# Optimization experiments

Hardware: AMD Instinct MI355X
Metric: run time of the kernel (lower is better)

Reference implementation:

```python
import jax, jax.numpy as jnp
import numpy as np

T, B = 384, 128
IN_DIM, HID, OUT_DIM = 512, 1024, 512


def _lstm_step(h, c, x_t, Wx, Wh, b):
    # x_t: [B, D], h/c: [B, H]; gates order: i, f, g, o
    gates = x_t @ Wx + h @ Wh + b  # [B, 4H]
    i, f, g, o = jnp.split(gates, 4, axis=-1)
    c_new = jax.nn.sigmoid(f) * c + jax.nn.sigmoid(i) * jnp.tanh(g)
    h_new = jax.nn.sigmoid(o) * jnp.tanh(c_new)
    return h_new, c_new


def setup_inputs() -> dict:
    key = jax.random.key(0)
    ks = jax.random.split(key, 9)
    s_in = 1.0 / np.sqrt(IN_DIM)
    s_h = 1.0 / np.sqrt(HID)
    s_o = 1.0 / np.sqrt(OUT_DIM)
    return {
        "x": jax.random.normal(ks[0], (T, B, IN_DIM), dtype=jnp.float32),
        "hidden_state": jnp.zeros((1, B, HID), dtype=jnp.float32),
        "cell_state": jnp.zeros((1, B, HID), dtype=jnp.float32),
        "enc_Wx": jax.random.normal(ks[1], (IN_DIM, 4 * HID), dtype=jnp.float32) * s_in,
        "enc_Wh": jax.random.normal(ks[2], (HID, 4 * HID), dtype=jnp.float32) * s_h,
        "enc_b": jnp.zeros((4 * HID,), dtype=jnp.float32),
        "dec_Wx": jax.random.normal(ks[3], (OUT_DIM, 4 * HID), dtype=jnp.float32) * s_o,
        "dec_Wh": jax.random.normal(ks[4], (HID, 4 * HID), dtype=jnp.float32) * s_h,
        "dec_b": jnp.zeros((4 * HID,), dtype=jnp.float32),
        "fc_W": jax.random.normal(ks[5], (HID, OUT_DIM), dtype=jnp.float32) * s_h,
        "fc_b": jnp.zeros((OUT_DIM,), dtype=jnp.float32),
    }


def reference(x, hidden_state, cell_state, enc_Wx, enc_Wh, enc_b,
              dec_Wx, dec_Wh, dec_b, fc_W, fc_b):
    # ---- encoder: run LSTM over T steps, keep only final hidden state ----
    h0, c0 = hidden_state[0], cell_state[0]  # [B, H]

    def enc_step(carry, x_t):
        h, c = carry
        h, c = _lstm_step(h, c, x_t, enc_Wx, enc_Wh, enc_b)
        return (h, c), None

    (h_enc, _), _ = jax.lax.scan(enc_step, (h0, c0), x)

    y0 = jnp.zeros((B, OUT_DIM), dtype=x.dtype)
    c_dec0 = jnp.zeros((B, HID), dtype=x.dtype)

    def dec_step(carry, _):
        y, h, c = carry
        h, c = _lstm_step(h, c, y, dec_Wx, dec_Wh, dec_b)
        y = jax.nn.softmax(h @ fc_W + fc_b, axis=-1)  # softmax over dim=2
        return (y, h, c), y

    _, output = jax.lax.scan(dec_step, (y0, h_enc, c_dec0), None, length=T)
    return output  # [T, B, OUT_DIM]
```

## Files before the change

### kernel.cpp

```cpp
#include <hip/hip_runtime.h>


#define TS 384

typedef __attribute__((ext_vector_type(8))) short bf16x8;
typedef __attribute__((ext_vector_type(4))) float f32x4;

#define WS_XR 4096u
#define XR_SLOT 262144u
#define WS_HP (WS_XR + 4u*XR_SLOT)
#define HP_BUF 524288u
#define WS_FPN (WS_HP + 2u*HP_BUF)
#define WS_TOTAL (WS_FPN + 2097152u)

__device__ __forceinline__ unsigned short bf16r(float v) {
  unsigned u = __float_as_uint(v);
  u += 0x7FFFu + ((u >> 16) & 1u);
  return (unsigned short)(u >> 16);
}
__device__ __forceinline__ float bf2f(unsigned short h) {
  return __uint_as_float(((unsigned)h) << 16);
}
__device__ __forceinline__ void split2(float v, short& hi, short& lo) {
  unsigned short h = bf16r(v);
  float r = v - bf2f(h);
  hi = (short)h; lo = (short)bf16r(r);
}
__device__ __forceinline__ float sigm(float v)  { return 1.0f / (1.0f + __expf(-v)); }
__device__ __forceinline__ float tanhfa(float v){ return 1.0f - 2.0f / (__expf(2.0f*v) + 1.0f); }

__device__ __forceinline__ void st_u64(void* p, unsigned long long v) {
  __hip_atomic_store((unsigned long long*)p, v, __ATOMIC_RELAXED, __HIP_MEMORY_SCOPE_AGENT);
}
__device__ __forceinline__ void st_f32(float* p, float v) {
  __hip_atomic_store(p, v, __ATOMIC_RELAXED, __HIP_MEMORY_SCOPE_AGENT);
}
__device__ __forceinline__ float ld_f32(const float* p) {
  return __hip_atomic_load(p, __ATOMIC_RELAXED, __HIP_MEMORY_SCOPE_AGENT);
}
union FRAG { unsigned long long q[2]; bf16x8 v; };
__device__ __forceinline__ bf16x8 ld_frag(const short* base) {
  FRAG u;
  u.q[0] = __hip_atomic_load((const unsigned long long*)base, __ATOMIC_RELAXED, __HIP_MEMORY_SCOPE_AGENT);
  u.q[1] = __hip_atomic_load((const unsigned long long*)(base + 4), __ATOMIC_RELAXED, __HIP_MEMORY_SCOPE_AGENT);
  return u.v;
}

__device__ __forceinline__ void setflag(unsigned* flag, unsigned val) {
  asm volatile("s_waitcnt vmcnt(0)" ::: "memory");
  __syncthreads();
  if (threadIdx.x == 0) {
    __hip_atomic_store(flag, val, __ATOMIC_RELAXED, __HIP_MEMORY_SCOPE_AGENT);
    asm volatile("s_waitcnt vmcnt(0)" ::: "memory");
  }
}
__device__ __forceinline__ void waitflags(const unsigned* flags, int nflags,
                                          unsigned target, bool fence, int* sDead) {
  if (threadIdx.x < 64) {
    const int i = threadIdx.x;
    const bool act = (i * 4) < nflags;
    const unsigned long long* q = (const unsigned long long*)(flags + i * 4);
    unsigned spins = 0;
    for (;;) {
      bool ok = true;
      if (act) {
        unsigned long long q0 = __hip_atomic_load(q, __ATOMIC_RELAXED, __HIP_MEMORY_SCOPE_AGENT);
        unsigned long long q1 = __hip_atomic_load(q + 1, __ATOMIC_RELAXED, __HIP_MEMORY_SCOPE_AGENT);
        ok = ((unsigned)q0 >= target) && ((unsigned)(q0 >> 32) >= target)
          && ((unsigned)q1 >= target) && ((unsigned)(q1 >> 32) >= target);
      }
      if (__all(ok)) break;
      __builtin_amdgcn_s_sleep(1);
      if (++spins > (1u << 19)) { if (i == 0) *sDead = 1; break; }
    }
    if (fence) __builtin_amdgcn_fence(__ATOMIC_ACQUIRE, "agent");
  }
  __syncthreads();
}

__device__ void load_gate_weights(const float* __restrict__ Wx, const float* __restrict__ Wh,
                                  int p, short* sBh, short* sBl) {
  for (int idx = threadIdx.x; idx < 24576; idx += 1024) {
    int j = idx & 7, l = (idx >> 3) & 63, kb = idx >> 9;
    int k = kb * 32 + ((l >> 4) << 3) + j;
    int c = l & 15;
    int gcol = (c >> 2) * 1024 + p * 4 + (c & 3);
    float wv = (k < 512) ? Wx[(size_t)k * 4096 + gcol]
                         : Wh[(size_t)(k - 512) * 4096 + gcol];
    short hi, lo; split2(wv, hi, lo);
    sBh[idx] = hi; sBl[idx] = lo;
  }
}
__device__ void load_fc_weights(const float* __restrict__ fcW, int kg, int cg,
                                short* sFh, short* sFl) {
  for (int idx = threadIdx.x; idx < 4096; idx += 1024) {
    int j = idx & 7, l = (idx >> 3) & 63, kb = idx >> 9;
    int unit = kg * 256 + kb * 32 + ((l >> 4) << 3) + j;
    int col = cg * 16 + (l & 15);
    short hi, lo; split2(fcW[(size_t)unit * 512 + col], hi, lo);
    sFh[idx] = hi; sFl[idx] = lo;
  }
}

__device__ __forceinline__ void gg(const short* AHs, const short* ALs,
    const short* BHs, const short* BLs, int mt, int l,
    int kbA0, int kbB0, int nkb, f32x4* acc)
{
  const bf16x8* AH = (const bf16x8*)AHs;
  const bf16x8* AL = (const bf16x8*)ALs;
  const bf16x8* BH = (const bf16x8*)BHs;
  const bf16x8* BL = (const bf16x8*)BLs;
  #pragma unroll 2
  for (int i = 0; i < nkb; i += 2) {
    int ka = kbA0 + i, kb = kbB0 + i;
    bf16x8 ah0 = AH[(ka * 8 + mt) * 64 + l];
    bf16x8 al0 = AL[(ka * 8 + mt) * 64 + l];
    bf16x8 bh0 = BH[kb * 64 + l];
    bf16x8 bl0 = BL[kb * 64 + l];
    bf16x8 ah1 = AH[((ka + 1) * 8 + mt) * 64 + l];
    bf16x8 al1 = AL[((ka + 1) * 8 + mt) * 64 + l];
    bf16x8 bh1 = BH[(kb + 1) * 64 + l];
    bf16x8 bl1 = BL[(kb + 1) * 64 + l];
    acc[0] = __builtin_amdgcn_mfma_f32_16x16x32_bf16(ah0, bh0, acc[0], 0, 0, 0);
    acc[1] = __builtin_amdgcn_mfma_f32_16x16x32_bf16(ah0, bl0, acc[1], 0, 0, 0);
    acc[2] = __builtin_amdgcn_mfma_f32_16x16x32_bf16(al0, bh0, acc[2], 0, 0, 0);
    acc[3] = __builtin_amdgcn_mfma_f32_16x16x32_bf16(ah1, bh1, acc[3], 0, 0, 0);
    acc[4] = __builtin_amdgcn_mfma_f32_16x16x32_bf16(ah1, bl1, acc[4], 0, 0, 0);
    acc[5] = __builtin_amdgcn_mfma_f32_16x16x32_bf16(al1, bh1, acc[5], 0, 0, 0);
  }
}
__device__ __forceinline__ void gg_finish(f32x4* acc, int kh, int mt, int l,
                                          float* LDSgate) {
  f32x4 s = (acc[0] + acc[3]) + ((acc[1] + acc[4]) + (acc[2] + acc[5]));
  const int col = l & 15, r0 = mt * 16 + ((l >> 4) << 2);
  float* plane = LDSgate + kh * 2176;
  #pragma unroll
  for (int j = 0; j < 4; ++j) plane[(r0 + j) * 17 + col] = s[j];
}

__device__ __forceinline__ void conv_x(const float* __restrict__ xsrc,
                                       short* dstH, short* dstL, int p, int t) {
  if (t < 32) {
    int g = p * 32 + t;
    int l = g & 63, mt = (g >> 6) & 7, kb = g >> 9;
    int row = mt * 16 + (l & 15), k = kb * 32 + ((l >> 4) << 3);
    const float* xs = xsrc + (size_t)row * 512 + k;
    unsigned long long h64[2] = {0, 0}, l64[2] = {0, 0};
    #pragma unroll
    for (int j = 0; j < 8; ++j) {
      short hi, lo; split2(xs[j], hi, lo);
      h64[j >> 2] |= (unsigned long long)(unsigned short)hi << ((j & 3) * 16);
      l64[j >> 2] |= (unsigned long long)(unsigned short)lo << ((j & 3) * 16);
    }
    int off = g * 8;
    st_u64(dstH + off, h64[0]); st_u64(dstH + off + 4, h64[1]);
    st_u64(dstL + off, l64[0]); st_u64(dstL + off + 4, l64[1]);
  }
}

__global__ void __launch_bounds__(1024, 1)
lstm6(const float* __restrict__ x, const float* __restrict__ h0p,
      const float* __restrict__ c0p, const float* __restrict__ eWx,
      const float* __restrict__ eWh, const float* __restrict__ eb,
      const float* __restrict__ dWx, const float* __restrict__ dWh,
      const float* __restrict__ db, const float* __restrict__ fcW,
      const float* __restrict__ fcb, float* __restrict__ out,
      char* __restrict__ ws)
{
  __shared__ __align__(16) short sBh[24576], sBl[24576];
  __shared__ __align__(16) short sFh[4096], sFl[4096];
  __shared__ float LDSgate[2 * 2176];
  __shared__ unsigned hsplit[512];
  __shared__ float ybuf[512];
  __shared__ float red[16];
  __shared__ int sDead;

  const int p = blockIdx.x, t = threadIdx.x;
  const int w = t >> 6, l = t & 63;
  const int mt = w & 7, kh = w >> 3;
  if (t == 0) sDead = 0;

  unsigned* hflag = (unsigned*)ws;
  unsigned* yflag = (unsigned*)(ws + 1024);
  unsigned* fflag = (unsigned*)(ws + 2048);

  short* xrH[4]; short* xrL[4];
  #pragma unroll
  for (int s4 = 0; s4 < 4; ++s4) {
    xrH[s4] = (short*)(ws + WS_XR + s4 * XR_SLOT);
    xrL[s4] = (short*)(ws + WS_XR + s4 * XR_SLOT + 131072u);
  }
  short* hpH[2]; short* hpL[2];
  #pragma unroll
  for (int b2 = 0; b2 < 2; ++b2) {
    hpH[b2] = (short*)(ws + WS_HP + b2 * HP_BUF);
    hpL[b2] = (short*)(ws + WS_HP + b2 * HP_BUF + 262144u);
  }
  float* fp = (float*)(ws + WS_FPN);

  const int row_pw = t & 127, u_pw = (t >> 7) & 3;

  load_gate_weights(eWx, eWh, p, sBh, sBl);
  conv_x(x, xrH[0], xrL[0], p, t);
  conv_x(x + 65536, xrH[1], xrL[1], p, t);
  if (t < 64) {
    int hg = p * 64 + t;
    int ll = hg & 63, mtt = (hg >> 6) & 7, hk = hg >> 9;
    int row = mtt * 16 + (ll & 15), k = hk * 32 + ((ll >> 4) << 3);
    const float* hs = h0p + (size_t)row * 1024 + k;
    unsigned long long h64[2] = {0, 0}, l64[2] = {0, 0};
    #pragma unroll
    for (int j = 0; j < 8; ++j) {
      short hi, lo; split2(hs[j], hi, lo);
      h64[j >> 2] |= (unsigned long long)(unsigned short)hi << ((j & 3) * 16);
      l64[j >> 2] |= (unsigned long long)(unsigned short)lo << ((j & 3) * 16);
    }
    int off = hg * 8;
    st_u64(hpH[0] + off, h64[0]); st_u64(hpH[0] + off + 4, h64[1]);
    st_u64(hpL[0] + off, l64[0]); st_u64(hpL[0] + off + 4, l64[1]);
  }
  float creg = 0.f, bq0 = 0.f, bq1 = 0.f, bq2 = 0.f, bq3 = 0.f;
  if (t < 512) {
    creg = c0p[(size_t)row_pw * 1024 + p * 4 + u_pw];
    bq0 = eb[0 * 1024 + p * 4 + u_pw];
    bq1 = eb[1 * 1024 + p * 4 + u_pw];
    bq2 = eb[2 * 1024 + p * 4 + u_pw];
    bq3 = eb[3 * 1024 + p * 4 + u_pw];
  }
  setflag(&hflag[p], 1u);
  waitflags(hflag, 256, 1u, true, &sDead);
  if (sDead) return;

  for (int st = 0; st < TS; ++st) {
    int rb = st & 1, wb = rb ^ 1, xs = st & 3;
    f32x4 z = {0.f, 0.f, 0.f, 0.f};
    f32x4 acc[6] = {z, z, z, z, z, z};
    gg(xrH[xs], xrL[xs], sBh, sBl, mt, l, kh * 8, kh * 8, 8, acc);
    waitflags(hflag, 256, (unsigned)(st + 1), true, &sDead);
    if (sDead) return;
    gg(hpH[rb], hpL[rb], sBh, sBl, mt, l, kh * 16, 16 + kh * 16, 16, acc);
    gg_finish(acc, kh, mt, l, LDSgate);
    __syncthreads();
    if (t < 512) {
      float g0 = LDSgate[row_pw * 17 + 0  + u_pw] + LDSgate[2176 + row_pw * 17 + 0  + u_pw] + bq0;
      float g1 = LDSgate[row_pw * 17 + 4  + u_pw] + LDSgate[2176 + row_pw * 17 + 4  + u_pw] + bq1;
      float g2 = LDSgate[row_pw * 17 + 8  + u_pw] + LDSgate[2176 + row_pw * 17 + 8  + u_pw] + bq2;
      float g3 = LDSgate[row_pw * 17 + 12 + u_pw] + LDSgate[2176 + row_pw * 17 + 12 + u_pw] + bq3;
      creg = sigm(g1) * creg + sigm(g0) * tanhfa(g2);
      float h = sigm(g3) * tanhfa(creg);
      short hi, lo; split2(h, hi, lo);
      hsplit[u_pw * 128 + row_pw] = ((unsigned)(unsigned short)hi << 16) | (unsigned short)lo;
    }
    if (st + 2 < TS)
      conv_x(x + (size_t)(st + 2) * 65536, xrH[(st + 2) & 3], xrL[(st + 2) & 3], p, t);
    __syncthreads();
    if (t < 128) {
      int r = t;
      unsigned w0 = hsplit[r], w1 = hsplit[128 + r], w2 = hsplit[256 + r], w3 = hsplit[384 + r];
      unsigned long long hi64 = (unsigned long long)(w0 >> 16)
        | ((unsigned long long)(w1 >> 16) << 16)
        | ((unsigned long long)(w2 >> 16) << 32)
        | ((unsigned long long)(w3 >> 16) << 48);
      unsigned long long lo64 = (unsigned long long)(w0 & 0xFFFFu)
        | ((unsigned long long)(w1 & 0xFFFFu) << 16)
        | ((unsigned long long)(w2 & 0xFFFFu) << 32)
        | ((unsigned long long)(w3 & 0xFFFFu) << 48);
      int hk = p >> 3, mtt = r >> 4;
      int lane_ = (((p >> 1) & 3) << 4) | (r & 15);
      int off = ((hk * 8 + mtt) * 64 + lane_) * 8 + (p & 1) * 4;
      st_u64(hpH[wb] + off, hi64);
      st_u64(hpL[wb] + off, lo64);
    }
    setflag(&hflag[p], (unsigned)(st + 2));
  }

  load_gate_weights(dWx, dWh, p, sBh, sBl);
  if (p >= 128) load_fc_weights(fcW, (p - 128) >> 5, (p - 128) & 31, sFh, sFl);
  if (t < 32) {
    int off = (p * 32 + t) * 8;
    st_u64(xrH[0] + off, 0ull); st_u64(xrH[0] + off + 4, 0ull);
    st_u64(xrL[0] + off, 0ull); st_u64(xrL[0] + off + 4, 0ull);
  }
  creg = 0.0f;
  if (t < 512) {
    bq0 = db[0 * 1024 + p * 4 + u_pw];
    bq1 = db[1 * 1024 + p * 4 + u_pw];
    bq2 = db[2 * 1024 + p * 4 + u_pw];
    bq3 = db[3 * 1024 + p * 4 + u_pw];
  }
  float fcb_r = (t < 512) ? fcb[t] : 0.f;
  setflag(&hflag[p], (unsigned)(TS + 2));

  const unsigned DB = (unsigned)(TS + 2);
  for (int st = 0; st < TS; ++st) {
    int rb = st & 1, wb = rb ^ 1;
    int ys = st & 1, yw = ys ^ 1;
    f32x4 z = {0.f, 0.f, 0.f, 0.f};
    f32x4 acc[6] = {z, z, z, z, z, z};
    waitflags(hflag, 256, DB + (unsigned)st, true, &sDead);
    if (sDead) return;
    gg(hpH[rb], hpL[rb], sBh, sBl, mt, l, kh * 16, 16 + kh * 16, 16, acc);
    waitflags(yflag, 128, (unsigned)st, false, &sDead);
    if (sDead) return;
    gg(xrH[ys], xrL[ys], sBh, sBl, mt, l, kh * 8, kh * 8, 8, acc);
    gg_finish(acc, kh, mt, l, LDSgate);
    __syncthreads();
    if (t < 512) {
      float g0 = LDSgate[row_pw * 17 + 0  + u_pw] + LDSgate[2176 + row_pw * 17 + 0  + u_pw] + bq0;
      float g1 = LDSgate[row_pw * 17 + 4  + u_pw] + LDSgate[2176 + row_pw * 17 + 4  + u_pw] + bq1;
      float g2 = LDSgate[row_pw * 17 + 8  + u_pw] + LDSgate[2176 + row_pw * 17 + 8  + u_pw] + bq2;
      float g3 = LDSgate[row_pw * 17 + 12 + u_pw] + LDSgate[2176 + row_pw * 17 + 12 + u_pw] + bq3;
      creg = sigm(g1) * creg + sigm(g0) * tanhfa(g2);
      float h = sigm(g3) * tanhfa(creg);
      short hi, lo; split2(h, hi, lo);
      hsplit[u_pw * 128 + row_pw] = ((unsigned)(unsigned short)hi << 16) | (unsigned short)lo;
    }
    __syncthreads();
    if (t < 128) {
      int r = t;
      unsigned w0 = hsplit[r], w1 = hsplit[128 + r], w2 = hsplit[256 + r], w3 = hsplit[384 + r];
      unsigned long long hi64 = (unsigned long long)(w0 >> 16)
        | ((unsigned long long)(w1 >> 16) << 16)
        | ((unsigned long long)(w2 >> 16) << 32)
        | ((unsigned long long)(w3 >> 16) << 48);
      unsigned long long lo64 = (unsigned long long)(w0 & 0xFFFFu)
        | ((unsigned long long)(w1 & 0xFFFFu) << 16)
        | ((unsigned long long)(w2 & 0xFFFFu) << 32)
        | ((unsigned long long)(w3 & 0xFFFFu) << 48);
      int hk = p >> 3, mtt = r >> 4;
      int lane_ = (((p >> 1) & 3) << 4) | (r & 15);
      int off = ((hk * 8 + mtt) * 64 + lane_) * 8 + (p & 1) * 4;
      st_u64(hpH[wb] + off, hi64);
      st_u64(hpL[wb] + off, lo64);
    }
    setflag(&hflag[p], DB + (unsigned)(st + 1));

    if (p >= 128) {
      const int f = p - 128, kg = f >> 5, cg = f & 31;
      waitflags(hflag + kg * 64, 64, DB + (unsigned)(st + 1), false, &sDead);
      if (sDead) return;
      {
        const bf16x8* FB = (const bf16x8*)sFh;
        const bf16x8* FL = (const bf16x8*)sFl;
        f32x4 a0 = z, a1 = z, a2 = z;
        #pragma unroll
        for (int kb = 0; kb < 4; ++kb) {
          int gkb = kg * 8 + kh * 4 + kb;
          bf16x8 ah = ld_frag(hpH[wb] + ((gkb * 8 + mt) * 64 + l) * 8);
          bf16x8 al = ld_frag(hpL[wb] + ((gkb * 8 + mt) * 64 + l) * 8);
          bf16x8 bh = FB[(kh * 4 + kb) * 64 + l];
          bf16x8 bl = FL[(kh * 4 + kb) * 64 + l];
          a0 = __builtin_amdgcn_mfma_f32_16x16x32_bf16(ah, bh, a0, 0, 0, 0);
          a1 = __builtin_amdgcn_mfma_f32_16x16x32_bf16(ah, bl, a1, 0, 0, 0);
          a2 = __builtin_amdgcn_mfma_f32_16x16x32_bf16(al, bh, a2, 0, 0, 0);
        }
        f32x4 s = a0 + (a1 + a2);
        int slice = kg * 2 + kh;
        int col = cg * 16 + (l & 15), r0 = mt * 16 + ((l >> 4) << 2);
        #pragma unroll
        for (int j = 0; j < 4; ++j)
          st_f32(&fp[(size_t)(slice * 128 + r0 + j) * 512 + col], s[j]);
      }
      setflag(&fflag[f], (unsigned)(st + 1));
    } else {
      waitflags(fflag, 128, (unsigned)(st + 1), false, &sDead);
      if (sDead) return;
      float v = 0.f, e = 0.f, mx;
      if (t < 512) {
        v = fcb_r;
        #pragma unroll
        for (int s8 = 0; s8 < 8; ++s8)
          v += ld_f32(&fp[(size_t)(s8 * 128 + p) * 512 + t]);
        mx = v;
        #pragma unroll
        for (int o = 32; o > 0; o >>= 1) mx = fmaxf(mx, __shfl_xor(mx, o));
        if (l == 0) red[w] = mx;
      }
      __syncthreads();
      if (t < 512) {
        mx = red[0];
        #pragma unroll
        for (int i = 1; i < 8; ++i) mx = fmaxf(mx, red[i]);
        e = __expf(v - mx);
        float ss = e;
        #pragma unroll
        for (int o = 32; o > 0; o >>= 1) ss += __shfl_xor(ss, o);
        if (l == 0) red[8 + w] = ss;
      }
      __syncthreads();
      if (t < 512) {
        float ss = (red[8] + red[9]) + (red[10] + red[11])
                 + (red[12] + red[13]) + (red[14] + red[15]);
        float y = e / ss;
        out[((size_t)st * 128 + p) * 512 + t] = y;
        ybuf[t] = y;
      }
      __syncthreads();
      if (t < 64) {
        int kb = t >> 2, seg = t & 3;
        int k = kb * 32 + seg * 8;
        int lane_ = (seg << 4) | (p & 15), mtt = p >> 4;
        int off = ((kb * 8 + mtt) * 64 + lane_) * 8;
        unsigned long long h64[2] = {0, 0}, l64[2] = {0, 0};
        #pragma unroll
        for (int j = 0; j < 8; ++j) {
          short hi, lo; split2(ybuf[k + j], hi, lo);
          h64[j >> 2] |= (unsigned long long)(unsigned short)hi << ((j & 3) * 16);
          l64[j >> 2] |= (unsigned long long)(unsigned short)lo << ((j & 3) * 16);
        }
        st_u64(xrH[yw] + off, h64[0]); st_u64(xrH[yw] + off + 4, h64[1]);
        st_u64(xrL[yw] + off, l64[0]); st_u64(xrL[yw] + off + 4, l64[1]);
      }
      setflag(&yflag[p], (unsigned)(st + 1));
    }
  }
}

extern "C" void kernel_launch(void* const* d_in, const int* in_sizes, int n_in,
                              void* d_out, int out_size, void* d_ws, size_t ws_size,
                              hipStream_t stream) {
  const float* x   = (const float*)d_in[0];
  const float* h0  = (const float*)d_in[1];
  const float* c0  = (const float*)d_in[2];
  const float* eWx = (const float*)d_in[3];
  const float* eWh = (const float*)d_in[4];
  const float* eb  = (const float*)d_in[5];
  const float* dWx = (const float*)d_in[6];
  const float* dWh = (const float*)d_in[7];
  const float* db  = (const float*)d_in[8];
  const float* fcW = (const float*)d_in[9];
  const float* fcb = (const float*)d_in[10];
  float* out = (float*)d_out;

  if (ws_size < (size_t)WS_TOTAL) {
    hipMemsetAsync(d_out, 0xFF, (size_t)out_size * sizeof(float), stream);
    return;
  }
  hipMemsetAsync(d_ws, 0, 4096, stream);
  hipLaunchKernelGGL(lstm6, dim3(256), dim3(1024), 0, stream,
                     x, h0, c0, eWx, eWh, eb, dWx, dWh, db, fcW, fcb, out,
                     (char*)d_ws);
}
```

Measured before the change: 15.77 ms.

## Use hierarchical flag aggregation for grid barriers and pipeline MFMA operand loads

Replaces the flat wait, where every block polls all 256 (or 128) flags, with a two-level scheme. A few designated aggregator blocks poll a 32-flag group each and publish one summary flag, and all blocks then poll only the 4–8 summary words. This cuts global polling traffic on every step's cross-block barrier. The GEMM inner loop is rewritten as a templated, fully unrolled software pipeline that prefetches A fragments a few k-blocks ahead. The FC stage batches its global fragment loads before the MFMAs. The x-conversion work moves to the threads that are otherwise idle during the gate nonlinearity, and the partial-sum reduction becomes a tree. The aggregation adds an extra hop of latency per barrier and depends on the aggregator blocks making progress.

After: 16.65 ms. +5.6%, slower.

```diff
diff --git a/kernel.cpp b/kernel.cpp
--- a/kernel.cpp
+++ b/kernel.cpp
@@ -13,6 +13,8 @@
 #define WS_FPN (WS_HP + 2u*HP_BUF)
 #define WS_TOTAL (WS_FPN + 2097152u)
 
+#define MFMA __builtin_amdgcn_mfma_f32_16x16x32_bf16
+
 __device__ __forceinline__ unsigned short bf16r(float v) {
   unsigned u = __float_as_uint(v);
   u += 0x7FFFu + ((u >> 16) & 1u);
@@ -32,6 +34,12 @@
 __device__ __forceinline__ void st_u64(void* p, unsigned long long v) {
   __hip_atomic_store((unsigned long long*)p, v, __ATOMIC_RELAXED, __HIP_MEMORY_SCOPE_AGENT);
 }
+__device__ __forceinline__ unsigned long long ld_u64(const void* p) {
+  return __hip_atomic_load((const unsigned long long*)p, __ATOMIC_RELAXED, __HIP_MEMORY_SCOPE_AGENT);
+}
+__device__ __forceinline__ void st_u32(unsigned* p, unsigned v) {
+  __hip_atomic_store(p, v, __ATOMIC_RELAXED, __HIP_MEMORY_SCOPE_AGENT);
+}
 __device__ __forceinline__ void st_f32(float* p, float v) {
   __hip_atomic_store(p, v, __ATOMIC_RELAXED, __HIP_MEMORY_SCOPE_AGENT);
 }
@@ -41,39 +49,66 @@
 union FRAG { unsigned long long q[2]; bf16x8 v; };
 __device__ __forceinline__ bf16x8 ld_frag(const short* base) {
   FRAG u;
-  u.q[0] = __hip_atomic_load((const unsigned long long*)base, __ATOMIC_RELAXED, __HIP_MEMORY_SCOPE_AGENT);
-  u.q[1] = __hip_atomic_load((const unsigned long long*)(base + 4), __ATOMIC_RELAXED, __HIP_MEMORY_SCOPE_AGENT);
+  u.q[0] = ld_u64(base);
+  u.q[1] = ld_u64(base + 4);
   return u.v;
 }
 
 __device__ __forceinline__ void setflag(unsigned* flag, unsigned val) {
   asm volatile("s_waitcnt vmcnt(0)" ::: "memory");
   __syncthreads();
-  if (threadIdx.x == 0) {
+  if (threadIdx.x == 0)
     __hip_atomic_store(flag, val, __ATOMIC_RELAXED, __HIP_MEMORY_SCOPE_AGENT);
-    asm volatile("s_waitcnt vmcnt(0)" ::: "memory");
-  }
-}
-__device__ __forceinline__ void waitflags(const unsigned* flags, int nflags,
-                                          unsigned target, bool fence, int* sDead) {
-  if (threadIdx.x < 64) {
-    const int i = threadIdx.x;
-    const bool act = (i * 4) < nflags;
-    const unsigned long long* q = (const unsigned long long*)(flags + i * 4);
+}
+__device__ __forceinline__ void wait_hier(const unsigned* flags, unsigned* pub,
+    int aggIdx, int nPub, unsigned target, bool fence, int* sDead) {
+  const int t = threadIdx.x;
+  if (aggIdx >= 0) {
+    if (t < 8) {
+      const unsigned long long* q = (const unsigned long long*)(flags + aggIdx * 32 + t * 4);
+      unsigned spins = 0;
+      for (;;) {
+        unsigned long long q0 = ld_u64(q), q1 = ld_u64(q + 1);
+        bool ok = ((unsigned)q0 >= target) && ((unsigned)(q0 >> 32) >= target)
+               && ((unsigned)q1 >= target) && ((unsigned)(q1 >> 32) >= target);
+        if (__all(ok)) break;
+        __builtin_amdgcn_s_sleep(1);
+        if (++spins > (1u << 19)) { if (t == 0) *sDead = 1; break; }
+      }
+    }
+    if (t == 0) st_u32(&pub[aggIdx], target);
+  }
+  if (t == 0) {
     unsigned spins = 0;
     for (;;) {
       bool ok = true;
-      if (act) {
-        unsigned long long q0 = __hip_atomic_load(q, __ATOMIC_RELAXED, __HIP_MEMORY_SCOPE_AGENT);
-        unsigned long long q1 = __hip_atomic_load(q + 1, __ATOMIC_RELAXED, __HIP_MEMORY_SCOPE_AGENT);
-        ok = ((unsigned)q0 >= target) && ((unsigned)(q0 >> 32) >= target)
-          && ((unsigned)q1 >= target) && ((unsigned)(q1 >> 32) >= target);
-      }
+      #pragma unroll
+      for (int i = 0; i < 4; ++i) {
+        if (i * 2 < nPub) {
+          unsigned long long q0 = ld_u64((const unsigned long long*)pub + i);
+          if (!((unsigned)q0 >= target && (unsigned)(q0 >> 32) >= target)) ok = false;
+        }
+      }
+      if (ok) break;
+      __builtin_amdgcn_s_sleep(1);
+      if (++spins > (1u << 19)) { *sDead = 1; break; }
+    }
+    if (fence) __builtin_amdgcn_fence(__ATOMIC_ACQUIRE, "agent");
+  }
+  __syncthreads();
+}
+__device__ __forceinline__ void wait64(const unsigned* flags, unsigned target, int* sDead) {
+  if (threadIdx.x < 16) {
+    const unsigned long long* q = (const unsigned long long*)(flags + threadIdx.x * 4);
+    unsigned spins = 0;
+    for (;;) {
+      unsigned long long q0 = ld_u64(q), q1 = ld_u64(q + 1);
+      bool ok = ((unsigned)q0 >= target) && ((unsigned)(q0 >> 32) >= target)
+             && ((unsigned)q1 >= target) && ((unsigned)(q1 >> 32) >= target);
       if (__all(ok)) break;
       __builtin_amdgcn_s_sleep(1);
-      if (++spins > (1u << 19)) { if (i == 0) *sDead = 1; break; }
-    }
-    if (fence) __builtin_amdgcn_fence(__ATOMIC_ACQUIRE, "agent");
+      if (++spins > (1u << 19)) { if (threadIdx.x == 0) *sDead = 1; break; }
+    }
   }
   __syncthreads();
 }
@@ -102,31 +137,34 @@
   }
 }
 
-__device__ __forceinline__ void gg(const short* AHs, const short* ALs,
-    const short* BHs, const short* BLs, int mt, int l,
-    int kbA0, int kbB0, int nkb, f32x4* acc)
+template<int NKB, int D>
+__device__ __forceinline__ void gg_pipe(const short* AH_, const short* AL_,
+    const short* BH_, const short* BL_, int mt, int l,
+    int kbA0, int kbB0, f32x4* acc)
 {
-  const bf16x8* AH = (const bf16x8*)AHs;
-  const bf16x8* AL = (const bf16x8*)ALs;
-  const bf16x8* BH = (const bf16x8*)BHs;
-  const bf16x8* BL = (const bf16x8*)BLs;
-  #pragma unroll 2
-  for (int i = 0; i < nkb; i += 2) {
-    int ka = kbA0 + i, kb = kbB0 + i;
-    bf16x8 ah0 = AH[(ka * 8 + mt) * 64 + l];
-    bf16x8 al0 = AL[(ka * 8 + mt) * 64 + l];
-    bf16x8 bh0 = BH[kb * 64 + l];
-    bf16x8 bl0 = BL[kb * 64 + l];
-    bf16x8 ah1 = AH[((ka + 1) * 8 + mt) * 64 + l];
-    bf16x8 al1 = AL[((ka + 1) * 8 + mt) * 64 + l];
-    bf16x8 bh1 = BH[(kb + 1) * 64 + l];
-    bf16x8 bl1 = BL[(kb + 1) * 64 + l];
-    acc[0] = __builtin_amdgcn_mfma_f32_16x16x32_bf16(ah0, bh0, acc[0], 0, 0, 0);
-    acc[1] = __builtin_amdgcn_mfma_f32_16x16x32_bf16(ah0, bl0, acc[1], 0, 0, 0);
-    acc[2] = __builtin_amdgcn_mfma_f32_16x16x32_bf16(al0, bh0, acc[2], 0, 0, 0);
-    acc[3] = __builtin_amdgcn_mfma_f32_16x16x32_bf16(ah1, bh1, acc[3], 0, 0, 0);
-    acc[4] = __builtin_amdgcn_mfma_f32_16x16x32_bf16(ah1, bl1, acc[4], 0, 0, 0);
-    acc[5] = __builtin_amdgcn_mfma_f32_16x16x32_bf16(al1, bh1, acc[5], 0, 0, 0);
+  const bf16x8* AH = (const bf16x8*)AH_;
+  const bf16x8* AL = (const bf16x8*)AL_;
+  const bf16x8* BH = (const bf16x8*)BH_;
+  const bf16x8* BL = (const bf16x8*)BL_;
+  bf16x8 pah[D], pal[D];
+  #pragma unroll
+  for (int i = 0; i < D; ++i) {
+    pah[i] = AH[((kbA0 + i) * 8 + mt) * 64 + l];
+    pal[i] = AL[((kbA0 + i) * 8 + mt) * 64 + l];
+  }
+  #pragma unroll
+  for (int i = 0; i < NKB; ++i) {
+    bf16x8 ah = pah[i % D], al = pal[i % D];
+    if (i + D < NKB) {
+      pah[i % D] = AH[((kbA0 + i + D) * 8 + mt) * 64 + l];
+      pal[i % D] = AL[((kbA0 + i + D) * 8 + mt) * 64 + l];
+    }
+    bf16x8 bh = BH[(kbB0 + i) * 64 + l];
+    bf16x8 bl = BL[(kbB0 + i) * 64 + l];
+    const int a = (i & 1) * 3;
+    acc[a + 0] = MFMA(ah, bh, acc[a + 0], 0, 0, 0);
+    acc[a + 1] = MFMA(ah, bl, acc[a + 1], 0, 0, 0);
+    acc[a + 2] = MFMA(al, bh, acc[a + 2], 0, 0, 0);
   }
 }
 __device__ __forceinline__ void gg_finish(f32x4* acc, int kh, int mt, int l,
@@ -139,9 +177,9 @@
 }
 
 __device__ __forceinline__ void conv_x(const float* __restrict__ xsrc,
-                                       short* dstH, short* dstL, int p, int t) {
-  if (t < 32) {
-    int g = p * 32 + t;
+                                       short* dstH, short* dstL, int p, int tl) {
+  if (tl < 32) {
+    int g = p * 32 + tl;
     int l = g & 63, mt = (g >> 6) & 7, kb = g >> 9;
     int row = mt * 16 + (l & 15), k = kb * 32 + ((l >> 4) << 3);
     const float* xs = xsrc + (size_t)row * 512 + k;
@@ -159,7 +197,7 @@
 }
 
 __global__ void __launch_bounds__(1024, 1)
-lstm6(const float* __restrict__ x, const float* __restrict__ h0p,
+lstm9(const float* __restrict__ x, const float* __restrict__ h0p,
       const float* __restrict__ c0p, const float* __restrict__ eWx,
       const float* __restrict__ eWh, const float* __restrict__ eb,
       const float* __restrict__ dWx, const float* __restrict__ dWh,
@@ -183,6 +221,13 @@
   unsigned* hflag = (unsigned*)ws;
   unsigned* yflag = (unsigned*)(ws + 1024);
   unsigned* fflag = (unsigned*)(ws + 2048);
+  unsigned* hpub  = (unsigned*)(ws + 3072);
+  unsigned* ypub  = (unsigned*)(ws + 3200);
+  unsigned* fpub  = (unsigned*)(ws + 3328);
+
+  const int hagg = (p < 8) ? p : -1;
+  const int yagg = (p >= 8 && p < 12) ? p - 8 : -1;
+  const int fagg = (p >= 12 && p < 16) ? p - 12 : -1;
 
   short* xrH[4]; short* xrL[4];
   #pragma unroll
@@ -228,17 +273,17 @@
     bq3 = eb[3 * 1024 + p * 4 + u_pw];
   }
   setflag(&hflag[p], 1u);
-  waitflags(hflag, 256, 1u, true, &sDead);
+  wait_hier(hflag, hpub, hagg, 8, 1u, true, &sDead);
   if (sDead) return;
 
   for (int st = 0; st < TS; ++st) {
     int rb = st & 1, wb = rb ^ 1, xs = st & 3;
     f32x4 z = {0.f, 0.f, 0.f, 0.f};
     f32x4 acc[6] = {z, z, z, z, z, z};
-    gg(xrH[xs], xrL[xs], sBh, sBl, mt, l, kh * 8, kh * 8, 8, acc);
-    waitflags(hflag, 256, (unsigned)(st + 1), true, &sDead);
+    gg_pipe<8, 4>(xrH[xs], xrL[xs], sBh, sBl, mt, l, kh * 8, kh * 8, acc);
+    wait_hier(hflag, hpub, hagg, 8, (unsigned)(st + 1), true, &sDead);
     if (sDead) return;
-    gg(hpH[rb], hpL[rb], sBh, sBl, mt, l, kh * 16, 16 + kh * 16, 16, acc);
+    gg_pipe<16, 4>(hpH[rb], hpL[rb], sBh, sBl, mt, l, kh * 16, 16 + kh * 16, acc);
     gg_finish(acc, kh, mt, l, LDSgate);
     __syncthreads();
     if (t < 512) {
@@ -250,9 +295,9 @@
       float h = sigm(g3) * tanhfa(creg);
       short hi, lo; split2(h, hi, lo);
       hsplit[u_pw * 128 + row_pw] = ((unsigned)(unsigned short)hi << 16) | (unsigned short)lo;
-    }
-    if (st + 2 < TS)
-      conv_x(x + (size_t)(st + 2) * 65536, xrH[(st + 2) & 3], xrL[(st + 2) & 3], p, t);
+    } else if (st + 2 < TS) {
+      conv_x(x + (size_t)(st + 2) * 65536, xrH[(st + 2) & 3], xrL[(st + 2) & 3], p, t - 512);
+    }
     __syncthreads();
     if (t < 128) {
       int r = t;
@@ -297,12 +342,12 @@
     int ys = st & 1, yw = ys ^ 1;
     f32x4 z = {0.f, 0.f, 0.f, 0.f};
     f32x4 acc[6] = {z, z, z, z, z, z};
-    waitflags(hflag, 256, DB + (unsigned)st, true, &sDead);
+    wait_hier(hflag, hpub, hagg, 8, DB + (unsigned)st, true, &sDead);
     if (sDead) return;
-    gg(hpH[rb], hpL[rb], sBh, sBl, mt, l, kh * 16, 16 + kh * 16, 16, acc);
-    waitflags(yflag, 128, (unsigned)st, false, &sDead);
+    gg_pipe<16, 4>(hpH[rb], hpL[rb], sBh, sBl, mt, l, kh * 16, 16 + kh * 16, acc);
+    wait_hier(yflag, ypub, yagg, 4, (unsigned)st, false, &sDead);
     if (sDead) return;
-    gg(xrH[ys], xrL[ys], sBh, sBl, mt, l, kh * 8, kh * 8, 8, acc);
+    gg_pipe<8, 4>(xrH[ys], xrL[ys], sBh, sBl, mt, l, kh * 8, kh * 8, acc);
     gg_finish(acc, kh, mt, l, LDSgate);
     __syncthreads();
     if (t < 512) {
@@ -337,22 +382,26 @@
 
     if (p >= 128) {
       const int f = p - 128, kg = f >> 5, cg = f & 31;
-      waitflags(hflag + kg * 64, 64, DB + (unsigned)(st + 1), false, &sDead);
+      wait64(hflag + kg * 64, DB + (unsigned)(st + 1), &sDead);
       if (sDead) return;
       {
         const bf16x8* FB = (const bf16x8*)sFh;
         const bf16x8* FL = (const bf16x8*)sFl;
-        f32x4 a0 = z, a1 = z, a2 = z;
+        bf16x8 fah[4], fal[4];
         #pragma unroll
         for (int kb = 0; kb < 4; ++kb) {
           int gkb = kg * 8 + kh * 4 + kb;
-          bf16x8 ah = ld_frag(hpH[wb] + ((gkb * 8 + mt) * 64 + l) * 8);
-          bf16x8 al = ld_frag(hpL[wb] + ((gkb * 8 + mt) * 64 + l) * 8);
+          fah[kb] = ld_frag(hpH[wb] + ((gkb * 8 + mt) * 64 + l) * 8);
+          fal[kb] = ld_frag(hpL[wb] + ((gkb * 8 + mt) * 64 + l) * 8);
+        }
+        f32x4 a0 = z, a1 = z, a2 = z;
+        #pragma unroll
+        for (int kb = 0; kb < 4; ++kb) {
           bf16x8 bh = FB[(kh * 4 + kb) * 64 + l];
           bf16x8 bl = FL[(kh * 4 + kb) * 64 + l];
-          a0 = __builtin_amdgcn_mfma_f32_16x16x32_bf16(ah, bh, a0, 0, 0, 0);
-          a1 = __builtin_amdgcn_mfma_f32_16x16x32_bf16(ah, bl, a1, 0, 0, 0);
-          a2 = __builtin_amdgcn_mfma_f32_16x16x32_bf16(al, bh, a2, 0, 0, 0);
+          a0 = MFMA(fah[kb], bh, a0, 0, 0, 0);
+          a1 = MFMA(fah[kb], bl, a1, 0, 0, 0);
+          a2 = MFMA(fal[kb], bh, a2, 0, 0, 0);
         }
         f32x4 s = a0 + (a1 + a2);
         int slice = kg * 2 + kh;
@@ -363,14 +412,16 @@
       }
       setflag(&fflag[f], (unsigned)(st + 1));
     } else {
-      waitflags(fflag, 128, (unsigned)(st + 1), false, &sDead);
+      wait_hier(fflag, fpub, fagg, 4, (unsigned)(st + 1), false, &sDead);
       if (sDead) return;
       float v = 0.f, e = 0.f, mx;
       if (t < 512) {
-        v = fcb_r;
+        float tv[8];
         #pragma unroll
         for (int s8 = 0; s8 < 8; ++s8)
-          v += ld_f32(&fp[(size_t)(s8 * 128 + p) * 512 + t]);
+          tv[s8] = ld_f32(&fp[(size_t)(s8 * 128 + p) * 512 + t]);
+        v = fcb_r + ((tv[0] + tv[1]) + (tv[2] + tv[3]))
+                  + ((tv[4] + tv[5]) + (tv[6] + tv[7]));
         mx = v;
         #pragma unroll
         for (int o = 32; o > 0; o >>= 1) mx = fmaxf(mx, __shfl_xor(mx, o));
@@ -437,7 +488,7 @@
     return;
   }
   hipMemsetAsync(d_ws, 0, 4096, stream);
-  hipLaunchKernelGGL(lstm6, dim3(256), dim3(1024), 0, stream,
+  hipLaunchKernelGGL(lstm9, dim3(256), dim3(1024), 0, stream,
                      x, h0, c0, eWx, eWh, eb, dWx, dWh, db, fcW, fcb, out,
                      (char*)d_ws);
 }
```
